# Kernel tuning notes

Measured on AMD Instinct MI355X. Metric: run time of the kernel, lower is better.

## Reference

```python
import jax, jax.numpy as jnp
import numpy as np

N = 50000
E = 800000
F_IN = 128
HID = 32
HEADS = 4
SLOPE = 0.2


def setup_inputs() -> dict:
    key = jax.random.key(0)
    ks = jax.random.split(key, 12)
    x = jax.random.normal(ks[0], (N, F_IN), dtype=jnp.float32)
    edge_index = jax.random.randint(ks[1], (2, E), 0, N, dtype=jnp.int64)
    edge_attr = jax.random.normal(ks[2], (E, 4), dtype=jnp.float32)
    s1 = 1.0 / np.sqrt(F_IN)
    s2 = 1.0 / np.sqrt(HID)
    W1 = jax.random.normal(ks[3], (F_IN, HEADS * HID), dtype=jnp.float32) * s1
    a_src1 = jax.random.normal(ks[4], (HEADS, HID), dtype=jnp.float32) * s2
    a_dst1 = jax.random.normal(ks[5], (HEADS, HID), dtype=jnp.float32) * s2
    b1 = jnp.zeros((HID,), dtype=jnp.float32)
    W2 = jax.random.normal(ks[6], (HID, 1), dtype=jnp.float32) * s2
    a_src2 = jax.random.normal(ks[7], (1, 1), dtype=jnp.float32)
    a_dst2 = jax.random.normal(ks[8], (1, 1), dtype=jnp.float32)
    b2 = jnp.zeros((1,), dtype=jnp.float32)
    return {"input_tensor": x, "edge_index": edge_index, "edge_attr": edge_attr,
            "W1": W1, "a_src1": a_src1, "a_dst1": a_dst1, "b1": b1,
            "W2": W2, "a_src2": a_src2, "a_dst2": a_dst2, "b2": b2}


def _gat_conv(x, src, dst, W, a_src, a_dst, b, heads, out_ch):
    n = x.shape[0]
    h = (x @ W).reshape(n, heads, out_ch)          # [N, H, C]
    alpha_src = jnp.sum(h * a_src, axis=-1)        # [N, H]
    alpha_dst = jnp.sum(h * a_dst, axis=-1)        # [N, H]
    e = alpha_src[src] + alpha_dst[dst]            # [E, H]
    e = jax.nn.leaky_relu(e, negative_slope=SLOPE)
    # segment softmax over edges grouped by destination node
    e_max = jax.ops.segment_max(e, dst, num_segments=n)
    e = jnp.exp(e - e_max[dst])
    denom = jax.ops.segment_sum(e, dst, num_segments=n)
    alpha = e / denom[dst]                         # [E, H]
    msg = h[src] * alpha[..., None]                # [E, H, C]
    out = jax.ops.segment_sum(msg, dst, num_segments=n)  # [N, H, C]
    return out.mean(axis=1) + b                    # concat=False -> mean over heads


def reference(input_tensor, edge_index, edge_attr, W1, a_src1, a_dst1, b1, W2, a_src2, a_dst2, b2):
    # PyG GATConv adds self-loops by default; edge_attr unused (edge_dim=None)
    loops = jnp.arange(N, dtype=edge_index.dtype)
    src = jnp.concatenate([edge_index[0], loops])
    dst = jnp.concatenate([edge_index[1], loops])
    x = _gat_conv(input_tensor, src, dst, W1, a_src1, a_dst1, b1, HEADS, HID)
    x = jax.nn.elu(x)
    x = _gat_conv(x, src, dst, W2, a_src2, a_dst2, b2, 1, 1)
    return x
```

## Files before the change

### kernel.cpp

```cpp
#include <hip/hip_runtime.h>
#include <hip/hip_fp16.h>
#include <math.h>
#include <stdint.h>

static constexpr int kN     = 50000;
static constexpr int kFIn   = 128;
static constexpr int kHeads = 4;
static constexpr int kScanB = 256;
static constexpr int kScanNB = (kN + kScanB - 1) / kScanB;
static constexpr int kGemmGrid = 782;

typedef _Float16 half8v  __attribute__((ext_vector_type(8)));
typedef float    floatx4 __attribute__((ext_vector_type(4)));

__device__ __forceinline__ float lrelu(float x) { return x > 0.f ? x : 0.2f * x; }

__device__ __forceinline__ float pack2h(float a, float b) {
    const __half2 h = __floats2half2_rn(a, b);
    return __uint_as_float(__builtin_bit_cast(uint32_t, h));
}

__global__ void k_init(int* __restrict__ p, int n) {
    int i = blockIdx.x * blockDim.x + threadIdx.x;
    if (i < n) p[i] = 0;
}

__global__ __launch_bounds__(256)
void k_gemm1_hist(const float* __restrict__ x, const float* __restrict__ W1,
                  __half* __restrict__ h1h, int nPass,
                  const int* __restrict__ ei, int E,
                  int* __restrict__ deg, int* __restrict__ rank) {
    __shared__ __align__(16) float whf[128 * 16 * 4];
    __shared__ __align__(16) float xsf[32 * 16 * 4];

    if (blockIdx.x >= kGemmGrid) {
        const int i = (blockIdx.x - kGemmGrid) * 256 + threadIdx.x;
        const int total = E + kN;
        if (i < total) {
            const int d = (i < E) ? ei[E + i] : (i - E);
            rank[i] = atomicAdd(&deg[d], 1);
        }
        return;
    }

    const int t = threadIdx.x;
    const int l = t & 63;
    const int g = t >> 6;
    for (int idx = t; idx < 2048; idx += 256) {
        const int c = idx >> 7, col = idx & 127;
        float4 st;
        st.x = pack2h(W1[(8 * c + 0) * 128 + col], W1[(8 * c + 1) * 128 + col]);
        st.y = pack2h(W1[(8 * c + 2) * 128 + col], W1[(8 * c + 3) * 128 + col]);
        st.z = pack2h(W1[(8 * c + 4) * 128 + col], W1[(8 * c + 5) * 128 + col]);
        st.w = pack2h(W1[(8 * c + 6) * 128 + col], W1[(8 * c + 7) * 128 + col]);
        const int gran = col * 16 + ((c + col) & 15);
        *reinterpret_cast<float4*>(&whf[gran * 4]) = st;
    }
    __syncthreads();

    const int rt  = g & 1;
    const int ctB = (g >> 1) * 4;
    const int lm  = l & 15;
    const int lk  = l >> 4;

    for (int pass = blockIdx.x; pass < nPass; pass += kGemmGrid) {
        const int nodeBase = pass * 32;
        for (int q = t; q < 512; q += 256) {
            const int nn = q >> 4, ck = q & 15;
            int n = nodeBase + nn; if (n >= kN) n = kN - 1;
            const float4 xa = *reinterpret_cast<const float4*>(&x[(size_t)n * 128 + ck * 8]);
            const float4 xb = *reinterpret_cast<const float4*>(&x[(size_t)n * 128 + ck * 8 + 4]);
            float4 st;
            st.x = pack2h(xa.x, xa.y);
            st.y = pack2h(xa.z, xa.w);
            st.z = pack2h(xb.x, xb.y);
            st.w = pack2h(xb.z, xb.w);
            const int gran = nn * 16 + ((ck + nn) & 15);
            *reinterpret_cast<float4*>(&xsf[gran * 4]) = st;
        }
        __syncthreads();

        floatx4 acc0 = {0.f, 0.f, 0.f, 0.f};
        floatx4 acc1 = {0.f, 0.f, 0.f, 0.f};
        floatx4 acc2 = {0.f, 0.f, 0.f, 0.f};
        floatx4 acc3 = {0.f, 0.f, 0.f, 0.f};
        const int node = rt * 16 + lm;
        const int ch0  = ctB * 16 + lm;
#pragma unroll
        for (int kk = 0; kk < 4; ++kk) {
            const int ck = lk + 4 * kk;
            const half8v af = *reinterpret_cast<const half8v*>(
                &xsf[(node * 16 + ((ck + node) & 15)) * 4]);
            const half8v b0 = *reinterpret_cast<const half8v*>(
                &whf[((ch0 +  0) * 16 + ((ck + ch0 +  0) & 15)) * 4]);
            const half8v b1 = *reinterpret_cast<const half8v*>(
                &whf[((ch0 + 16) * 16 + ((ck + ch0 + 16) & 15)) * 4]);
            const half8v b2 = *reinterpret_cast<const half8v*>(
                &whf[((ch0 + 32) * 16 + ((ck + ch0 + 32) & 15)) * 4]);
            const half8v b3 = *reinterpret_cast<const half8v*>(
                &whf[((ch0 + 48) * 16 + ((ck + ch0 + 48) & 15)) * 4]);
            acc0 = __builtin_amdgcn_mfma_f32_16x16x32_f16(af, b0, acc0, 0, 0, 0);
            acc1 = __builtin_amdgcn_mfma_f32_16x16x32_f16(af, b1, acc1, 0, 0, 0);
            acc2 = __builtin_amdgcn_mfma_f32_16x16x32_f16(af, b2, acc2, 0, 0, 0);
            acc3 = __builtin_amdgcn_mfma_f32_16x16x32_f16(af, b3, acc3, 0, 0, 0);
        }
        const int nrow0 = nodeBase + rt * 16 + lk * 4;
#pragma unroll
        for (int r = 0; r < 4; ++r) {
            const int n = nrow0 + r;
            if (n < kN) {
                h1h[(size_t)n * 128 + ch0     ] = __float2half(acc0[r]);
                h1h[(size_t)n * 128 + ch0 + 16] = __float2half(acc1[r]);
                h1h[(size_t)n * 128 + ch0 + 32] = __float2half(acc2[r]);
                h1h[(size_t)n * 128 + ch0 + 48] = __float2half(acc3[r]);
            }
        }
        __syncthreads();
    }
}

__global__ __launch_bounds__(256)
void k_logits_scana(const __half* __restrict__ h1h,
                    const float* __restrict__ a_src1, const float* __restrict__ a_dst1,
                    float* __restrict__ asrc, float* __restrict__ adst,
                    const int* __restrict__ deg, int* __restrict__ loc,
                    int* __restrict__ bsum) {
    __shared__ int tmp[kScanB];
    if (blockIdx.x < kScanNB) {
        const int t = threadIdx.x;
        const int i = blockIdx.x * kScanB + t;
        int v = (i < kN) ? deg[i] : 0;
        tmp[t] = v;
        __syncthreads();
        for (int off = 1; off < kScanB; off <<= 1) {
            int add = (t >= off) ? tmp[t - off] : 0;
            __syncthreads();
            tmp[t] += add;
            __syncthreads();
        }
        if (i < kN) loc[i] = tmp[t] - v;
        if (t == kScanB - 1) bsum[blockIdx.x] = tmp[t];
        return;
    }
    const int n = (blockIdx.x - kScanNB) * 4 + (threadIdx.x >> 6);
    if (n >= kN) return;
    const int j = threadIdx.x & 63;
    const float2 f = __half22float2(*(const __half2*)&h1h[(size_t)n * 128 + 2 * j]);
    float ps = f.x * a_src1[2 * j] + f.y * a_src1[2 * j + 1];
    float pd = f.x * a_dst1[2 * j] + f.y * a_dst1[2 * j + 1];
#pragma unroll
    for (int off = 8; off >= 1; off >>= 1) {
        ps += __shfl_xor(ps, off, 64);
        pd += __shfl_xor(pd, off, 64);
    }
    if ((j & 15) == 0) {
        asrc[n * 4 + (j >> 4)] = ps;
        adst[n * 4 + (j >> 4)] = pd;
    }
}

__global__ void k_scan_b(int* __restrict__ bsum) {
    __shared__ int tmp[256];
    int t = threadIdx.x;
    int v = (t < kScanNB) ? bsum[t] : 0;
    tmp[t] = v;
    __syncthreads();
    for (int off = 1; off < 256; off <<= 1) {
        int add = (t >= off) ? tmp[t - off] : 0;
        __syncthreads();
        tmp[t] += add;
        __syncthreads();
    }
    if (t < kScanNB) bsum[t] = tmp[t] - v;
}

__global__ void k_scan_c(const int* __restrict__ loc, const int* __restrict__ bsum,
                         int* __restrict__ rowptr, int E2) {
    int i = blockIdx.x * kScanB + threadIdx.x;
    if (i < kN) rowptr[i] = loc[i] + bsum[blockIdx.x];
    if (i == 0) rowptr[kN] = E2;
}

__global__ void k_scatter(const int* __restrict__ ei, int E,
                          const int* __restrict__ rowptr, const int* __restrict__ rank,
                          int* __restrict__ es) {
    int i = blockIdx.x * blockDim.x + threadIdx.x;
    int total = E + kN;
    if (i >= total) return;
    int s, d;
    if (i < E) { s = ei[i]; d = ei[E + i]; } else { s = d = i - E; }
    es[rowptr[d] + rank[i]] = s;
}

__global__ __launch_bounds__(256)
void k_wgt(const int* __restrict__ rowptr, const int* __restrict__ es,
           const float* __restrict__ asrc, const float* __restrict__ adst,
           __half* __restrict__ alphaH) {
    const int n = blockIdx.x * 16 + (threadIdx.x >> 4);
    if (n >= kN) return;
    const int l = threadIdx.x & 15;
    const int beg = rowptr[n], end = rowptr[n + 1];
    const float ad0 = adst[n * 4 + 0], ad1 = adst[n * 4 + 1];
    const float ad2 = adst[n * 4 + 2], ad3 = adst[n * 4 + 3];
    float t0 = 0.f, t1 = 0.f, t2 = 0.f, t3 = 0.f;
    for (int p = beg + l; p < end; p += 16) {
        const int s = es[p];
        t0 += expf(lrelu(asrc[s * 4 + 0] + ad0));
        t1 += expf(lrelu(asrc[s * 4 + 1] + ad1));
        t2 += expf(lrelu(asrc[s * 4 + 2] + ad2));
        t3 += expf(lrelu(asrc[s * 4 + 3] + ad3));
    }
#pragma unroll
    for (int off = 8; off >= 1; off >>= 1) {
        t0 += __shfl_xor(t0, off, 64);
        t1 += __shfl_xor(t1, off, 64);
        t2 += __shfl_xor(t2, off, 64);
        t3 += __shfl_xor(t3, off, 64);
    }
    const float r0 = 1.f / t0, r1 = 1.f / t1, r2 = 1.f / t2, r3 = 1.f / t3;
    for (int p = beg + l; p < end; p += 16) {
        const int s = es[p];
        const float w0 = expf(lrelu(asrc[s * 4 + 0] + ad0)) * r0;
        const float w1 = expf(lrelu(asrc[s * 4 + 1] + ad1)) * r1;
        const float w2 = expf(lrelu(asrc[s * 4 + 2] + ad2)) * r2;
        const float w3 = expf(lrelu(asrc[s * 4 + 3] + ad3)) * r3;
        float2 st;
        st.x = pack2h(w0, w1);
        st.y = pack2h(w2, w3);
        *reinterpret_cast<float2*>(&alphaH[(size_t)p * 4]) = st;
    }
}

__global__ __launch_bounds__(256)
void k_agg1(const int* __restrict__ rowptr, const int* __restrict__ es,
            const __half* __restrict__ alphaH,
            const __half* __restrict__ h1h, const float* __restrict__ b1,
            const float* __restrict__ W2, float* __restrict__ h2) {
    const int n = blockIdx.x * 4 + (threadIdx.x >> 6);
    if (n >= kN) return;
    const int j  = threadIdx.x & 63;
    const int hh = j >> 4;
    const int beg = rowptr[n], end = rowptr[n + 1];
    const __half2* h12 = (const __half2*)h1h;
    __half2 accA = __floats2half2_rn(0.f, 0.f);
    __half2 accB = __floats2half2_rn(0.f, 0.f);
    int p = beg;
    for (; p + 8 <= end; p += 8) {
        const int s0 = es[p],     s1 = es[p + 1];
        const int s2 = es[p + 2], s3 = es[p + 3];
        const int s4 = es[p + 4], s5 = es[p + 5];
        const int s6 = es[p + 6], s7 = es[p + 7];
        const __half a0 = alphaH[(p + 0) * 4 + hh];
        const __half a1 = alphaH[(p + 1) * 4 + hh];
        const __half a2 = alphaH[(p + 2) * 4 + hh];
        const __half a3 = alphaH[(p + 3) * 4 + hh];
        const __half a4 = alphaH[(p + 4) * 4 + hh];
        const __half a5 = alphaH[(p + 5) * 4 + hh];
        const __half a6 = alphaH[(p + 6) * 4 + hh];
        const __half a7 = alphaH[(p + 7) * 4 + hh];
        const __half2 v0 = h12[s0 * 64 + j];
        const __half2 v1 = h12[s1 * 64 + j];
        const __half2 v2 = h12[s2 * 64 + j];
        const __half2 v3 = h12[s3 * 64 + j];
        const __half2 v4 = h12[s4 * 64 + j];
        const __half2 v5 = h12[s5 * 64 + j];
        const __half2 v6 = h12[s6 * 64 + j];
        const __half2 v7 = h12[s7 * 64 + j];
        accA = __hfma2(__half2half2(a0), v0, accA);
        accB = __hfma2(__half2half2(a1), v1, accB);
        accA = __hfma2(__half2half2(a2), v2, accA);
        accB = __hfma2(__half2half2(a3), v3, accB);
        accA = __hfma2(__half2half2(a4), v4, accA);
        accB = __hfma2(__half2half2(a5), v5, accB);
        accA = __hfma2(__half2half2(a6), v6, accA);
        accB = __hfma2(__half2half2(a7), v7, accB);
    }
    for (; p + 4 <= end; p += 4) {
        const int s0 = es[p],     s1 = es[p + 1];
        const int s2 = es[p + 2], s3 = es[p + 3];
        const __half a0 = alphaH[(p + 0) * 4 + hh];
        const __half a1 = alphaH[(p + 1) * 4 + hh];
        const __half a2 = alphaH[(p + 2) * 4 + hh];
        const __half a3 = alphaH[(p + 3) * 4 + hh];
        const __half2 v0 = h12[s0 * 64 + j];
        const __half2 v1 = h12[s1 * 64 + j];
        const __half2 v2 = h12[s2 * 64 + j];
        const __half2 v3 = h12[s3 * 64 + j];
        accA = __hfma2(__half2half2(a0), v0, accA);
        accB = __hfma2(__half2half2(a1), v1, accB);
        accA = __hfma2(__half2half2(a2), v2, accA);
        accB = __hfma2(__half2half2(a3), v3, accB);
    }
    for (; p < end; ++p) {
        const int s0 = es[p];
        const __half a0 = alphaH[p * 4 + hh];
        accA = __hfma2(__half2half2(a0), h12[s0 * 64 + j], accA);
    }
    const float2 fa = __half22float2(accA);
    const float2 fb = __half22float2(accB);
    float vx = fa.x + fb.x;
    float vy = fa.y + fb.y;
    vx += __shfl_xor(vx, 32, 64); vy += __shfl_xor(vy, 32, 64);
    vx += __shfl_xor(vx, 16, 64); vy += __shfl_xor(vy, 16, 64);
    const int m = j & 15;
    float u0 = 0.25f * vx + b1[2 * m];
    float u1 = 0.25f * vy + b1[2 * m + 1];
    u0 = u0 > 0.f ? u0 : expf(u0) - 1.f;
    u1 = u1 > 0.f ? u1 : expf(u1) - 1.f;
    float tsum = u0 * W2[2 * m] + u1 * W2[2 * m + 1];
    tsum += __shfl_xor(tsum, 8, 64);
    tsum += __shfl_xor(tsum, 4, 64);
    tsum += __shfl_xor(tsum, 2, 64);
    tsum += __shfl_xor(tsum, 1, 64);
    if (j == 0) h2[n] = tsum;
}

__global__ __launch_bounds__(256)
void k_agg2(const int* __restrict__ rowptr, const int* __restrict__ es,
            const float* __restrict__ h2,
            const float* __restrict__ a_s2, const float* __restrict__ a_d2,
            const float* __restrict__ b2, float* __restrict__ out) {
    const int n = blockIdx.x * 16 + (threadIdx.x >> 4);
    if (n >= kN) return;
    const int l = threadIdx.x & 15;
    const float as = a_s2[0], ad = a_d2[0];
    const int beg = rowptr[n], end = rowptr[n + 1];
    const float hd = h2[n] * ad;
    float sw = 0.f, swh = 0.f;
    for (int p = beg + l; p < end; p += 16) {
        float hs = h2[es[p]];
        float w = expf(lrelu(hs * as + hd));
        sw += w;
        swh += w * hs;
    }
#pragma unroll
    for (int off = 8; off >= 1; off >>= 1) {
        sw  += __shfl_xor(sw, off, 64);
        swh += __shfl_xor(swh, off, 64);
    }
    if (l == 0) out[n] = swh / sw + b2[0];
}

extern "C" void kernel_launch(void* const* d_in, const int* in_sizes, int n_in,
                              void* d_out, int out_size, void* d_ws, size_t ws_size,
                              hipStream_t stream) {
    const float* x      = (const float*)d_in[0];
    const int*   ei     = (const int*)d_in[1];
    const float* W1     = (const float*)d_in[3];
    const float* a_src1 = (const float*)d_in[4];
    const float* a_dst1 = (const float*)d_in[5];
    const float* b1     = (const float*)d_in[6];
    const float* W2     = (const float*)d_in[7];
    const float* a_src2 = (const float*)d_in[8];
    const float* a_dst2 = (const float*)d_in[9];
    const float* b2     = (const float*)d_in[10];
    float* out = (float*)d_out;

    const int E  = in_sizes[1] / 2;
    const int E2 = E + kN;

    float*   ws     = (float*)d_ws;
    float*   asrc   = ws;
    float*   adst   = ws + 200000;
    float*   h2     = ws + 400000;
    __half*  h1h    = (__half*)(ws + 450000);
    __half*  alphaH = (__half*)(ws + 3650000);
    int*     ibase  = (int*)(ws + 5350000);
    int*     es     = ibase;
    int*     deg    = ibase + 850000;
    int*     rank   = ibase + 900000;
    int*     loc    = ibase + 1750000;
    int*     rowptr = ibase + 1800000;
    int*     bsum   = ibase + 1850016;

    k_init<<<(kN + 255) / 256, 256, 0, stream>>>(deg, kN);

    {
        const int nPass      = (kN + 31) / 32;
        const int histBlocks = (E2 + 255) / 256;
        k_gemm1_hist<<<kGemmGrid + histBlocks, 256, 0, stream>>>(
            x, W1, h1h, nPass, ei, E, deg, rank);
    }

    {
        const int logitBlocks = (kN + 3) / 4;
        k_logits_scana<<<kScanNB + logitBlocks, 256, 0, stream>>>(
            h1h, a_src1, a_dst1, asrc, adst, deg, loc, bsum);
    }

    k_scan_b<<<1, 256, 0, stream>>>(bsum);
    k_scan_c<<<kScanNB, kScanB, 0, stream>>>(loc, bsum, rowptr, E2);

    k_scatter<<<(E2 + 255) / 256, 256, 0, stream>>>(ei, E, rowptr, rank, es);

    k_wgt<<<(kN + 15) / 16, 256, 0, stream>>>(rowptr, es, asrc, adst, alphaH);

    k_agg1<<<(kN + 3) / 4, 256, 0, stream>>>(rowptr, es, alphaH, h1h, b1, W2, h2);

    k_agg2<<<(kN + 15) / 16, 256, 0, stream>>>(rowptr, es, h2, a_src2, a_dst2, b2, out);
}
```

Measured before the change: 131.0 us.

## Shard degree histogram atomics four ways and fuse block-sum scan into rowptr kernel

The per-destination degree counter is split into four shards chosen by edge index, which spreads atomic contention across more addresses. Per-node shard prefix offsets are stored and used in the scatter so the CSR ordering stays consistent. The separate single-block scan of block sums is removed: each rowptr block now rescans the small bsum array itself, which saves one launch at the cost of redundant work. Memory traffic rises somewhat because the init, scan and scatter read four shard arrays plus an int4 prefix per node.

```diff
diff --git a/kernel.cpp b/kernel.cpp
--- a/kernel.cpp
+++ b/kernel.cpp
@@ -29,7 +29,7 @@
 void k_gemm1_hist(const float* __restrict__ x, const float* __restrict__ W1,
                   __half* __restrict__ h1h, int nPass,
                   const int* __restrict__ ei, int E,
-                  int* __restrict__ deg, int* __restrict__ rank) {
+                  int* __restrict__ degS, int* __restrict__ rank) {
     __shared__ __align__(16) float whf[128 * 16 * 4];
     __shared__ __align__(16) float xsf[32 * 16 * 4];
 
@@ -38,7 +38,8 @@
         const int total = E + kN;
         if (i < total) {
             const int d = (i < E) ? ei[E + i] : (i - E);
-            rank[i] = atomicAdd(&deg[d], 1);
+            const int s = i & 3;
+            rank[i] = atomicAdd(&degS[s * kN + d], 1);
         }
         return;
     }
@@ -123,13 +124,28 @@
 void k_logits_scana(const __half* __restrict__ h1h,
                     const float* __restrict__ a_src1, const float* __restrict__ a_dst1,
                     float* __restrict__ asrc, float* __restrict__ adst,
-                    const int* __restrict__ deg, int* __restrict__ loc,
-                    int* __restrict__ bsum) {
+                    const int* __restrict__ degS, int* __restrict__ loc,
+                    int* __restrict__ bsum, int* __restrict__ shardPre) {
     __shared__ int tmp[kScanB];
     if (blockIdx.x < kScanNB) {
         const int t = threadIdx.x;
         const int i = blockIdx.x * kScanB + t;
-        int v = (i < kN) ? deg[i] : 0;
+        int d0 = 0, d1 = 0, d2 = 0, d3 = 0;
+        if (i < kN) {
+            d0 = degS[0 * kN + i];
+            d1 = degS[1 * kN + i];
+            d2 = degS[2 * kN + i];
+            d3 = degS[3 * kN + i];
+        }
+        const int v = d0 + d1 + d2 + d3;
+        if (i < kN) {
+            int4 pre;
+            pre.x = 0;
+            pre.y = d0;
+            pre.z = d0 + d1;
+            pre.w = d0 + d1 + d2;
+            reinterpret_cast<int4*>(shardPre)[i] = pre;
+        }
         tmp[t] = v;
         __syncthreads();
         for (int off = 1; off < kScanB; off <<= 1) {
@@ -159,9 +175,11 @@
     }
 }
 
-__global__ void k_scan_b(int* __restrict__ bsum) {
+__global__ void k_scan_c(const int* __restrict__ loc, const int* __restrict__ bsum,
+                         int* __restrict__ rowptr, int E2) {
     __shared__ int tmp[256];
-    int t = threadIdx.x;
+    const int t = threadIdx.x;
+    const int bid = blockIdx.x;
     int v = (t < kScanNB) ? bsum[t] : 0;
     tmp[t] = v;
     __syncthreads();
@@ -171,25 +189,24 @@
         tmp[t] += add;
         __syncthreads();
     }
-    if (t < kScanNB) bsum[t] = tmp[t] - v;
-}
-
-__global__ void k_scan_c(const int* __restrict__ loc, const int* __restrict__ bsum,
-                         int* __restrict__ rowptr, int E2) {
-    int i = blockIdx.x * kScanB + threadIdx.x;
-    if (i < kN) rowptr[i] = loc[i] + bsum[blockIdx.x];
+    const int S = (bid > 0) ? tmp[bid - 1] : 0;
+    const int i = bid * kScanB + t;
+    if (i < kN) rowptr[i] = loc[i] + S;
     if (i == 0) rowptr[kN] = E2;
 }
 
 __global__ void k_scatter(const int* __restrict__ ei, int E,
                           const int* __restrict__ rowptr, const int* __restrict__ rank,
-                          int* __restrict__ es) {
+                          const int* __restrict__ shardPre, int* __restrict__ es) {
     int i = blockIdx.x * blockDim.x + threadIdx.x;
     int total = E + kN;
     if (i >= total) return;
     int s, d;
     if (i < E) { s = ei[i]; d = ei[E + i]; } else { s = d = i - E; }
-    es[rowptr[d] + rank[i]] = s;
+    const int4 pre = reinterpret_cast<const int4*>(shardPre)[d];
+    const int sh = i & 3;
+    const int off = (sh == 0) ? pre.x : (sh == 1) ? pre.y : (sh == 2) ? pre.z : pre.w;
+    es[rowptr[d] + off + rank[i]] = s;
 }
 
 __global__ __launch_bounds__(256)
@@ -359,39 +376,39 @@
     const int E  = in_sizes[1] / 2;
     const int E2 = E + kN;
 
-    float*   ws     = (float*)d_ws;
-    float*   asrc   = ws;
-    float*   adst   = ws + 200000;
-    float*   h2     = ws + 400000;
-    __half*  h1h    = (__half*)(ws + 450000);
-    __half*  alphaH = (__half*)(ws + 3650000);
-    int*     ibase  = (int*)(ws + 5350000);
-    int*     es     = ibase;
-    int*     deg    = ibase + 850000;
-    int*     rank   = ibase + 900000;
-    int*     loc    = ibase + 1750000;
-    int*     rowptr = ibase + 1800000;
-    int*     bsum   = ibase + 1850016;
-
-    k_init<<<(kN + 255) / 256, 256, 0, stream>>>(deg, kN);
+    float*   ws       = (float*)d_ws;
+    float*   asrc     = ws;
+    float*   adst     = ws + 200000;
+    float*   h2       = ws + 400000;
+    __half*  h1h      = (__half*)(ws + 450000);
+    __half*  alphaH   = (__half*)(ws + 3650000);
+    int*     ibase    = (int*)(ws + 5350000);
+    int*     es       = ibase;
+    int*     degS     = ibase + 850000;
+    int*     rank     = ibase + 1050000;
+    int*     loc      = ibase + 1900000;
+    int*     rowptr   = ibase + 1950000;
+    int*     bsum     = ibase + 2000016;
+    int*     shardPre = ibase + 2000288;
+
+    k_init<<<(4 * kN + 255) / 256, 256, 0, stream>>>(degS, 4 * kN);
 
     {
         const int nPass      = (kN + 31) / 32;
         const int histBlocks = (E2 + 255) / 256;
         k_gemm1_hist<<<kGemmGrid + histBlocks, 256, 0, stream>>>(
-            x, W1, h1h, nPass, ei, E, deg, rank);
+            x, W1, h1h, nPass, ei, E, degS, rank);
     }
 
     {
         const int logitBlocks = (kN + 3) / 4;
         k_logits_scana<<<kScanNB + logitBlocks, 256, 0, stream>>>(
-            h1h, a_src1, a_dst1, asrc, adst, deg, loc, bsum);
-    }
-
-    k_scan_b<<<1, 256, 0, stream>>>(bsum);
+            h1h, a_src1, a_dst1, asrc, adst, degS, loc, bsum, shardPre);
+    }
+
     k_scan_c<<<kScanNB, kScanB, 0, stream>>>(loc, bsum, rowptr, E2);
 
-    k_scatter<<<(E2 + 255) / 256, 256, 0, stream>>>(ei, E, rowptr, rank, es);
+    k_scatter<<<(E2 + 255) / 256, 256, 0, stream>>>(ei, E, rowptr, rank, shardPre, es);
 
     k_wgt<<<(kN + 15) / 16, 256, 0, stream>>>(rowptr, es, asrc, adst, alphaH);
 
```

Measured after the change: 137.7 us. +5.1%, slower.
